# Optimization experiments

Hardware: AMD Instinct MI355X
Metric: run time of the kernel (lower is better)

Reference implementation:

```python
import jax, jax.numpy as jnp
import numpy as np

B, T, C, H = 8, 2048, 1024, 64  # batch, seq (== block_size), n_embd, head_size


def setup_inputs() -> dict:
    key = jax.random.key(0)
    k1, k2, k3, k4 = jax.random.split(key, 4)
    x = jax.random.normal(k1, (B, T, C), dtype=jnp.float32)
    scale = 0.02
    Wk = jax.random.normal(k2, (H, C), dtype=jnp.float32) * scale  # nn.Linear weight [out,in]
    Wq = jax.random.normal(k3, (H, C), dtype=jnp.float32) * scale
    Wv = jax.random.normal(k4, (H, C), dtype=jnp.float32) * scale
    return {"x": x, "Wk": Wk, "Wq": Wq, "Wv": Wv}


def reference(x, Wk, Wq, Wv):
    # k, q, v projections (bias-free linears): x @ W.T
    k = jnp.einsum('btc,hc->bth', x, Wk)
    q = jnp.einsum('btc,hc->bth', x, Wq)
    v = jnp.einsum('btc,hc->bth', x, Wv)
    # NOTE: source MULTIPLIES by sqrt(head_size) (faithful to original code)
    wei = jnp.einsum('bth,bsh->bts', q, k) * (H ** 0.5)  # [B,T,T]
    causal = jnp.tril(jnp.ones((T, T), dtype=bool))
    wei = jnp.where(causal, wei, -jnp.inf)
    wei = jax.nn.softmax(wei, axis=-1)
    # dropout_value = 0.0 -> identity (deterministic baseline)
    out = jnp.einsum('bts,bsh->bth', wei, v)  # [B,T,H]
    return out
```

## Files before the change

kernel.cpp:

```cpp
#include <hip/hip_runtime.h>

#define BB 8
#define TT 2048
#define CC 1024
#define HH 64
#define MM (BB * TT)

typedef _Float16 half8 __attribute__((ext_vector_type(8)));
typedef _Float16 half4 __attribute__((ext_vector_type(4)));
typedef float floatx4 __attribute__((ext_vector_type(4)));

template <int CTRL>
__device__ __forceinline__ float dpp_max_step(float x)
{
    union { float f; int i; } u, v;
    u.f = x;
    v.i = __builtin_amdgcn_update_dpp(u.i, u.i, CTRL, 0xf, 0xf, false);
    return fmaxf(x, v.f);
}
__device__ __forceinline__ float rowmax16(float x)
{
    x = dpp_max_step<0x128>(x);
    x = dpp_max_step<0x124>(x);
    x = dpp_max_step<0x122>(x);
    x = dpp_max_step<0x121>(x);
    return x;
}

__device__ __forceinline__ void gll16(const float* g, float* l)
{
    __builtin_amdgcn_global_load_lds(
        (const __attribute__((address_space(1))) unsigned int*)g,
        (__attribute__((address_space(3))) unsigned int*)l, 16, 0, 0);
}
__device__ __forceinline__ void gll16h(const _Float16* g, _Float16* l)
{
    __builtin_amdgcn_global_load_lds(
        (const __attribute__((address_space(1))) unsigned int*)g,
        (__attribute__((address_space(3))) unsigned int*)l, 16, 0, 0);
}

#define MEMFENCE asm volatile("" ::: "memory")

__global__ __launch_bounds__(256)
void w_pack(const float* __restrict__ Wk, const float* __restrict__ Wq,
            const float* __restrict__ Wv, _Float16* __restrict__ Wp)
{
    const int T   = blockIdx.x * 256 + threadIdx.x;
    const int c   = T / 768;
    const int rem = T - c * 768;
    const int nf  = rem >> 6;
    const int l   = rem & 63;
    const int col = nf * 16 + (l & 15);
    const int k   = c * 32 + (l >> 4) * 8;
    const int which = col >> 6;
    const float* __restrict__ src = (which == 0) ? Wq : ((which == 1) ? Wk : Wv);
    const float scale = (which == 0) ? 8.0f : 1.0f;
    const int srow = col & 63;
    const float4 a = *reinterpret_cast<const float4*>(&src[srow * 1024 + k]);
    const float4 b = *reinterpret_cast<const float4*>(&src[srow * 1024 + k + 4]);
    const half8 o = { (_Float16)(a.x * scale), (_Float16)(a.y * scale),
                      (_Float16)(a.z * scale), (_Float16)(a.w * scale),
                      (_Float16)(b.x * scale), (_Float16)(b.y * scale),
                      (_Float16)(b.z * scale), (_Float16)(b.w * scale) };
    *reinterpret_cast<half8*>(&Wp[(size_t)T * 8]) = o;
}

__global__ __launch_bounds__(512, 1)
void qkv12(const float* __restrict__ x, const _Float16* __restrict__ Wp,
           _Float16* __restrict__ q16, _Float16* __restrict__ Kp,
           _Float16* __restrict__ Vp)
{
    __shared__ float    xs[3][64][32];
    __shared__ _Float16 Ws[3][6144];

    const int tid  = threadIdx.x;
    const int lane = tid & 63;
    const int w    = tid >> 6;
    const int blk  = blockIdx.x;
    const int skew = blk & 31;
    const int m_base = blk * 64;
    const int fm = lane & 15;
    const int fq = lane >> 4;
    const int fk = fq * 8;
    const int fr = fq * 4;
    const int wm = w >> 2;
    const int wn = w & 3;

    const float* gsrc = &x[(size_t)(m_base + w * 8 + (lane >> 3)) * CC
                           + ((lane & 7) ^ (lane >> 3)) * 4];
    float* xbase = &xs[0][w * 8][0];

    const _Float16* wsrc = Wp + lane * 8;

    floatx4 acc[2][3];
    #pragma unroll
    for (int a = 0; a < 2; ++a)
        #pragma unroll
        for (int n = 0; n < 3; ++n)
            #pragma unroll
            for (int r = 0; r < 4; ++r) acc[a][n][r] = 0.0f;

#define STAGE_X(p, slot) gll16(gsrc + (size_t)(p) * 32, xbase + (slot) * 2048)
#define STAGE_W(p, slot) do {                                                  \
        const _Float16* wsp = wsrc + (size_t)(p) * 6144;                       \
        if (w < 4) {                                                           \
            gll16h(wsp + (2 * w) * 512,     &Ws[slot][(2 * w) * 512]);         \
            gll16h(wsp + (2 * w + 1) * 512, &Ws[slot][(2 * w + 1) * 512]);     \
        } else {                                                               \
            gll16h(wsp + (4 + w) * 512,     &Ws[slot][(4 + w) * 512]);         \
        }                                                                      \
    } while (0)

#define COMPUTE(sc) do {                                                       \
        const half8 wf0 = *reinterpret_cast<const half8*>(                     \
            &Ws[sc][(wn * 3 + 0) * 512 + lane * 8]);                           \
        const half8 wf1 = *reinterpret_cast<const half8*>(                     \
            &Ws[sc][(wn * 3 + 1) * 512 + lane * 8]);                           \
        const half8 wf2 = *reinterpret_cast<const half8*>(                     \
            &Ws[sc][(wn * 3 + 2) * 512 + lane * 8]);                           \
        _Pragma("unroll")                                                      \
        for (int a = 0; a < 2; ++a) {                                          \
            const float* rowp = &xs[sc][wm * 32 + a * 16 + fm][0];             \
            const int sw = fm & 7;                                             \
            const float4 v0 = *reinterpret_cast<const float4*>(                \
                rowp + ((fq * 2 + 0) ^ sw) * 4);                               \
            const float4 v1 = *reinterpret_cast<const float4*>(                \
                rowp + ((fq * 2 + 1) ^ sw) * 4);                               \
            const half8 af = { (_Float16)v0.x, (_Float16)v0.y,                 \
                               (_Float16)v0.z, (_Float16)v0.w,                 \
                               (_Float16)v1.x, (_Float16)v1.y,                 \
                               (_Float16)v1.z, (_Float16)v1.w };               \
            acc[a][0] = __builtin_amdgcn_mfma_f32_16x16x32_f16(af, wf0, acc[a][0], 0, 0, 0); \
            acc[a][1] = __builtin_amdgcn_mfma_f32_16x16x32_f16(af, wf1, acc[a][1], 0, 0, 0); \
            acc[a][2] = __builtin_amdgcn_mfma_f32_16x16x32_f16(af, wf2, acc[a][2], 0, 0, 0); \
        }                                                                      \
    } while (0)

#define WAITB(NLO, NHI) do {                                                   \
        if (w < 4) asm volatile("s_waitcnt vmcnt(" #NLO ")" ::: "memory");     \
        else       asm volatile("s_waitcnt vmcnt(" #NHI ")" ::: "memory");     \
        __builtin_amdgcn_s_barrier();                                          \
        MEMFENCE;                                                              \
    } while (0)

    MEMFENCE;
    STAGE_W(skew, 0);               STAGE_X(skew, 0);
    STAGE_W((skew + 1) & 31, 1);    STAGE_X((skew + 1) & 31, 1);
    WAITB(3, 2);

    for (int c = 0; c < 30; ++c) {
        const int pp = (c + 2 + skew) & 31;
        const int sl = (c + 2) % 3;
        STAGE_W(pp, sl);
        STAGE_X(pp, sl);
        MEMFENCE;
        COMPUTE(c % 3);
        WAITB(3, 2);
    }
    COMPUTE(0);
    WAITB(0, 0);
    COMPUTE(1);

#undef STAGE_X
#undef STAGE_W
#undef COMPUTE
#undef WAITB

    #pragma unroll
    for (int a = 0; a < 2; ++a) {
        const int mt = blk * 4 + wm * 2 + a;
        #pragma unroll
        for (int n = 0; n < 3; ++n) {
            const int col = wn * 48 + n * 16 + fm;
            if (col < 64) {
                #pragma unroll
                for (int r = 0; r < 4; ++r)
                    q16[(size_t)(mt * 16 + fr + r) * HH + col] = (_Float16)acc[a][n][r];
            } else if (col < 128) {
                const int h = col - 64;
                _Float16* kp = &Kp[(size_t)(mt * 2 + (h >> 5)) * 512 + (h & 31)];
                #pragma unroll
                for (int r = 0; r < 4; ++r)
                    kp[(fr + r) * 32] = (_Float16)acc[a][n][r];
            } else {
                const int h = col - 128;
                const half4 pk = { (_Float16)acc[a][n][0], (_Float16)acc[a][n][1],
                                   (_Float16)acc[a][n][2], (_Float16)acc[a][n][3] };
                *reinterpret_cast<half4*>(
                    &Vp[(size_t)((mt >> 2) * 4 + (h >> 4)) * 1024 +
                        ((mt >> 1) & 1) * 512 + fm * 32 + (mt & 1) * 16 + fr]) = pk;
            }
        }
    }
}

__global__ __launch_bounds__(256, 3)
void attn8(const _Float16* __restrict__ q16, const _Float16* __restrict__ Kp,
           const _Float16* __restrict__ Vp, float* __restrict__ out,
           _Float16* __restrict__ Op, float* __restrict__ ml)
{
    __shared__ _Float16 Kls[2][4][1024];
    __shared__ _Float16 Vls[2][4][1024];
    __shared__ _Float16 Ps[4][16 * 68];

    const int bid = blockIdx.x;
    const int g   = 31 - bid / 24;
    const int sub = bid - (31 - g) * 24;
    const int b   = sub & 7;
    const int s   = sub >> 3;

    const int tid  = threadIdx.x;
    const int lane = tid & 63;
    const int w    = tid >> 6;
    const int it   = g * 4 + w;
    const int fm = lane & 15;
    const int fq = lane >> 4;
    const int fk = fq * 8;
    const int fr = fq * 4;

    const int Ji = g + 1;
    const int qq = Ji / 3, rem = Ji - qq * 3;
    const int cnt   = qq + (s < rem ? 1 : 0);
    const int start = s * qq + (s < rem ? s : rem);

    const _Float16* __restrict__ kpb = Kp + (size_t)b * TT * HH;
    const _Float16* __restrict__ vpb = Vp + (size_t)b * TT * HH;

    const int qrow = (b * 128 + it) * 16 + fm;
    const half8 qf0 = *reinterpret_cast<const half8*>(&q16[(size_t)qrow * HH + fk]);
    const half8 qf1 = *reinterpret_cast<const half8*>(&q16[(size_t)qrow * HH + 32 + fk]);

    floatx4 O[4], lacc;
    float m_r[4];
    #pragma unroll
    for (int r = 0; r < 4; ++r) {
        m_r[r] = -3.0e38f;
        lacc[r] = 0.0f;
        #pragma unroll
        for (int ht = 0; ht < 4; ++ht) O[ht][r] = 0.0f;
    }
    const half8 ones = { (_Float16)1.f, (_Float16)1.f, (_Float16)1.f, (_Float16)1.f,
                         (_Float16)1.f, (_Float16)1.f, (_Float16)1.f, (_Float16)1.f };

    const int sperm = ((lane & 15) * 4 + (lane >> 4)) * 8;

    if (cnt > 0) {
        {
            const _Float16* kgp = &kpb[(size_t)(start * 4 + w) * 1024];
            const _Float16* vgp = &vpb[(size_t)(start * 4 + w) * 1024];
            gll16h(kgp + sperm,       &Kls[0][w][0]);
            gll16h(kgp + 512 + sperm, &Kls[0][w][512]);
            gll16h(vgp + sperm,       &Vls[0][w][0]);
            gll16h(vgp + 512 + sperm, &Vls[0][w][512]);
        }
        asm volatile("s_waitcnt vmcnt(0)" ::: "memory");
        __builtin_amdgcn_s_barrier();
        MEMFENCE;

        int buf = 0;
        for (int js = 0; js < cnt; ++js) {
            const int jj = start + js;

            if (js + 1 < cnt) {
                const _Float16* kgp = &kpb[(size_t)((jj + 1) * 4 + w) * 1024];
                const _Float16* vgp = &vpb[(size_t)((jj + 1) * 4 + w) * 1024];
                gll16h(kgp + sperm,       &Kls[buf ^ 1][w][0]);
                gll16h(kgp + 512 + sperm, &Kls[buf ^ 1][w][512]);
                gll16h(vgp + sperm,       &Vls[buf ^ 1][w][0]);
                gll16h(vgp + 512 + sperm, &Vls[buf ^ 1][w][512]);
            }
            MEMFENCE;

            floatx4 sa[4];
            #pragma unroll
            for (int nt = 0; nt < 4; ++nt) {
                #pragma unroll
                for (int r = 0; r < 4; ++r) sa[nt][r] = 0.0f;
                const half8 b0 = *reinterpret_cast<const half8*>(&Kls[buf][nt][lane * 8]);
                const half8 b1 = *reinterpret_cast<const half8*>(&Kls[buf][nt][512 + lane * 8]);
                sa[nt] = __builtin_amdgcn_mfma_f32_16x16x32_f16(qf0, b0, sa[nt], 0, 0, 0);
                sa[nt] = __builtin_amdgcn_mfma_f32_16x16x32_f16(qf1, b1, sa[nt], 0, 0, 0);
            }

            if (jj == g) {
                const int rbase = it * 16 + fr;
                #pragma unroll
                for (int nt = 0; nt < 4; ++nt) {
                    const int col = jj * 64 + nt * 16 + fm;
                    #pragma unroll
                    for (int r = 0; r < 4; ++r)
                        if (col > rbase + r) sa[nt][r] = -3.0e38f;
                }
            }

            #pragma unroll
            for (int r = 0; r < 4; ++r) {
                float mx = fmaxf(fmaxf(sa[0][r], sa[1][r]), fmaxf(sa[2][r], sa[3][r]));
                mx = rowmax16(mx);
                const float mn = fmaxf(m_r[r], mx);
                const float alpha = __expf(m_r[r] - mn);
                m_r[r] = mn;
                _Float16* pp = &Ps[w][(fr + r) * 68 + fm];
                pp[0]  = (_Float16)__expf(sa[0][r] - mn);
                pp[16] = (_Float16)__expf(sa[1][r] - mn);
                pp[32] = (_Float16)__expf(sa[2][r] - mn);
                pp[48] = (_Float16)__expf(sa[3][r] - mn);
                lacc[r] *= alpha;
                O[0][r] *= alpha; O[1][r] *= alpha; O[2][r] *= alpha; O[3][r] *= alpha;
            }

            #pragma unroll
            for (int ch = 0; ch < 2; ++ch) {
                const half8 pa = *reinterpret_cast<const half8*>(&Ps[w][fm * 68 + ch * 32 + fk]);
                lacc = __builtin_amdgcn_mfma_f32_16x16x32_f16(pa, ones, lacc, 0, 0, 0);
                #pragma unroll
                for (int ht = 0; ht < 4; ++ht) {
                    const half8 vb = *reinterpret_cast<const half8*>(
                        &Vls[buf][ht][ch * 512 + lane * 8]);
                    O[ht] = __builtin_amdgcn_mfma_f32_16x16x32_f16(pa, vb, O[ht], 0, 0, 0);
                }
            }

            asm volatile("s_waitcnt vmcnt(0)" ::: "memory");
            __builtin_amdgcn_s_barrier();
            MEMFENCE;
            buf ^= 1;
        }
    }

    #pragma unroll
    for (int r = 0; r < 4; ++r) {
        const int grow = (b * 128 + it) * 16 + fr + r;
        if (s == 0) {
            #pragma unroll
            for (int ht = 0; ht < 4; ++ht)
                out[(size_t)grow * HH + ht * 16 + fm] = O[ht][r];
        } else {
            #pragma unroll
            for (int ht = 0; ht < 4; ++ht)
                Op[((size_t)(s - 1) * MM + grow) * HH + ht * 16 + fm] = (_Float16)O[ht][r];
        }
        if (fm == 0) {
            ml[((size_t)s * MM + grow) * 2 + 0] = m_r[r];
            ml[((size_t)s * MM + grow) * 2 + 1] = lacc[r];
        }
    }
}

__global__ __launch_bounds__(256)
void combine(float* __restrict__ out, const _Float16* __restrict__ Op,
             const float* __restrict__ ml)
{
    const int tid  = threadIdx.x;
    const int grow = blockIdx.x * 64 + (tid >> 2);
    const int c0   = (tid & 3) * 16;

    const float m0 = ml[(size_t)grow * 2 + 0];
    const float l0 = ml[(size_t)grow * 2 + 1];
    const float m1 = ml[((size_t)MM + grow) * 2 + 0];
    const float l1 = ml[((size_t)MM + grow) * 2 + 1];
    const float m2 = ml[((size_t)2 * MM + grow) * 2 + 0];
    const float l2 = ml[((size_t)2 * MM + grow) * 2 + 1];

    const float M  = fmaxf(m0, fmaxf(m1, m2));
    const float w0 = __expf(m0 - M);
    const float w1 = __expf(m1 - M);
    const float w2 = __expf(m2 - M);
    const float inv = 1.0f / (w0 * l0 + w1 * l1 + w2 * l2);

    #pragma unroll
    for (int i = 0; i < 16; i += 4) {
        float4 o0 = *reinterpret_cast<float4*>(&out[(size_t)grow * HH + c0 + i]);
        const half4 h1 = *reinterpret_cast<const half4*>(&Op[(size_t)grow * HH + c0 + i]);
        const half4 h2 = *reinterpret_cast<const half4*>(&Op[(size_t)MM * HH + (size_t)grow * HH + c0 + i]);
        o0.x = (w0 * o0.x + w1 * (float)h1[0] + w2 * (float)h2[0]) * inv;
        o0.y = (w0 * o0.y + w1 * (float)h1[1] + w2 * (float)h2[1]) * inv;
        o0.z = (w0 * o0.z + w1 * (float)h1[2] + w2 * (float)h2[2]) * inv;
        o0.w = (w0 * o0.w + w1 * (float)h1[3] + w2 * (float)h2[3]) * inv;
        *reinterpret_cast<float4*>(&out[(size_t)grow * HH + c0 + i]) = o0;
    }
}

extern "C" void kernel_launch(void* const* d_in, const int* in_sizes, int n_in,
                              void* d_out, int out_size, void* d_ws, size_t ws_size,
                              hipStream_t stream)
{
    (void)in_sizes; (void)n_in; (void)out_size; (void)ws_size;

    const float* x  = (const float*)d_in[0];
    const float* Wk = (const float*)d_in[1];
    const float* Wq = (const float*)d_in[2];
    const float* Wv = (const float*)d_in[3];
    float* out = (float*)d_out;

    _Float16* base = (_Float16*)d_ws;
    _Float16* q16 = base;
    _Float16* Kp  = base + (size_t)MM * HH;
    _Float16* Vp  = base + (size_t)2 * MM * HH;
    _Float16* Wp  = base + (size_t)3 * MM * HH;
    _Float16* Op  = Wp + 192 * 1024;
    float*    ml  = (float*)(Op + (size_t)2 * MM * HH);

    w_pack<<<dim3(96), dim3(256), 0, stream>>>(Wk, Wq, Wv, Wp);
    qkv12<<<dim3(256), dim3(512), 0, stream>>>(x, Wp, q16, Kp, Vp);
    attn8<<<dim3(768), dim3(256), 0, stream>>>(q16, Kp, Vp, out, Op, ml);
    combine<<<dim3(256), dim3(256), 0, stream>>>(out, Op, ml);
}
```

Before: 146.9 us.

## Load x tiles directly into registers and double-buffer weights with 64-wide K steps

```diff
diff --git a/kernel.cpp b/kernel.cpp
--- a/kernel.cpp
+++ b/kernel.cpp
@@ -27,12 +27,6 @@
     return x;
 }
 
-__device__ __forceinline__ void gll16(const float* g, float* l)
-{
-    __builtin_amdgcn_global_load_lds(
-        (const __attribute__((address_space(1))) unsigned int*)g,
-        (__attribute__((address_space(3))) unsigned int*)l, 16, 0, 0);
-}
 __device__ __forceinline__ void gll16h(const _Float16* g, _Float16* l)
 {
     __builtin_amdgcn_global_load_lds(
@@ -67,18 +61,16 @@
 }
 
 __global__ __launch_bounds__(512, 1)
-void qkv12(const float* __restrict__ x, const _Float16* __restrict__ Wp,
+void qkv13(const float* __restrict__ x, const _Float16* __restrict__ Wp,
            _Float16* __restrict__ q16, _Float16* __restrict__ Kp,
            _Float16* __restrict__ Vp)
 {
-    __shared__ float    xs[3][64][32];
-    __shared__ _Float16 Ws[3][6144];
+    __shared__ _Float16 Ws[2][12288];
 
     const int tid  = threadIdx.x;
     const int lane = tid & 63;
     const int w    = tid >> 6;
     const int blk  = blockIdx.x;
-    const int skew = blk & 31;
     const int m_base = blk * 64;
     const int fm = lane & 15;
     const int fq = lane >> 4;
@@ -87,9 +79,8 @@
     const int wm = w >> 2;
     const int wn = w & 3;
 
-    const float* gsrc = &x[(size_t)(m_base + w * 8 + (lane >> 3)) * CC
-                           + ((lane & 7) ^ (lane >> 3)) * 4];
-    float* xbase = &xs[0][w * 8][0];
+    const float* xr0 = &x[(size_t)(m_base + wm * 32 + fm) * CC + fk];
+    const float* xr1 = xr0 + 16 * CC;
 
     const _Float16* wsrc = Wp + lane * 8;
 
@@ -101,71 +92,85 @@
             #pragma unroll
             for (int r = 0; r < 4; ++r) acc[a][n][r] = 0.0f;
 
-#define STAGE_X(p, slot) gll16(gsrc + (size_t)(p) * 32, xbase + (slot) * 2048)
-#define STAGE_W(p, slot) do {                                                  \
-        const _Float16* wsp = wsrc + (size_t)(p) * 6144;                       \
-        if (w < 4) {                                                           \
-            gll16h(wsp + (2 * w) * 512,     &Ws[slot][(2 * w) * 512]);         \
-            gll16h(wsp + (2 * w + 1) * 512, &Ws[slot][(2 * w + 1) * 512]);     \
-        } else {                                                               \
-            gll16h(wsp + (4 + w) * 512,     &Ws[slot][(4 + w) * 512]);         \
+    float4 xA[8], xB[8];
+
+#define STAGE_W(i, slot) do {                                                  \
+        const size_t fb = (size_t)(24 * (i) + 3 * w) * 512;                    \
+        gll16h(wsrc + fb,        &Ws[slot][(3 * w + 0) * 512]);                \
+        gll16h(wsrc + fb + 512,  &Ws[slot][(3 * w + 1) * 512]);                \
+        gll16h(wsrc + fb + 1024, &Ws[slot][(3 * w + 2) * 512]);                \
+    } while (0)
+
+#define LOAD_X(i, XB) do {                                                     \
+        _Pragma("unroll")                                                      \
+        for (int a = 0; a < 2; ++a) {                                          \
+            const float* xr = a ? xr1 : xr0;                                   \
+            _Pragma("unroll")                                                  \
+            for (int sub = 0; sub < 2; ++sub) {                                \
+                XB[a * 4 + sub * 2 + 0] = *reinterpret_cast<const float4*>(    \
+                    xr + (i) * 64 + sub * 32);                                 \
+                XB[a * 4 + sub * 2 + 1] = *reinterpret_cast<const float4*>(    \
+                    xr + (i) * 64 + sub * 32 + 4);                             \
+            }                                                                  \
         }                                                                      \
     } while (0)
 
-#define COMPUTE(sc) do {                                                       \
-        const half8 wf0 = *reinterpret_cast<const half8*>(                     \
-            &Ws[sc][(wn * 3 + 0) * 512 + lane * 8]);                           \
-        const half8 wf1 = *reinterpret_cast<const half8*>(                     \
-            &Ws[sc][(wn * 3 + 1) * 512 + lane * 8]);                           \
-        const half8 wf2 = *reinterpret_cast<const half8*>(                     \
-            &Ws[sc][(wn * 3 + 2) * 512 + lane * 8]);                           \
+#define COMPUTE(sl, XB) do {                                                   \
+        half8 wf[2][3];                                                        \
         _Pragma("unroll")                                                      \
-        for (int a = 0; a < 2; ++a) {                                          \
-            const float* rowp = &xs[sc][wm * 32 + a * 16 + fm][0];             \
-            const int sw = fm & 7;                                             \
-            const float4 v0 = *reinterpret_cast<const float4*>(                \
-                rowp + ((fq * 2 + 0) ^ sw) * 4);                               \
-            const float4 v1 = *reinterpret_cast<const float4*>(                \
-                rowp + ((fq * 2 + 1) ^ sw) * 4);                               \
-            const half8 af = { (_Float16)v0.x, (_Float16)v0.y,                 \
-                               (_Float16)v0.z, (_Float16)v0.w,                 \
-                               (_Float16)v1.x, (_Float16)v1.y,                 \
-                               (_Float16)v1.z, (_Float16)v1.w };               \
-            acc[a][0] = __builtin_amdgcn_mfma_f32_16x16x32_f16(af, wf0, acc[a][0], 0, 0, 0); \
-            acc[a][1] = __builtin_amdgcn_mfma_f32_16x16x32_f16(af, wf1, acc[a][1], 0, 0, 0); \
-            acc[a][2] = __builtin_amdgcn_mfma_f32_16x16x32_f16(af, wf2, acc[a][2], 0, 0, 0); \
-        }                                                                      \
+        for (int sub = 0; sub < 2; ++sub)                                      \
+            _Pragma("unroll")                                                  \
+            for (int n = 0; n < 3; ++n)                                        \
+                wf[sub][n] = *reinterpret_cast<const half8*>(                  \
+                    &Ws[sl][(sub * 12 + wn * 3 + n) * 512 + lane * 8]);        \
+        _Pragma("unroll")                                                      \
+        for (int a = 0; a < 2; ++a)                                            \
+            _Pragma("unroll")                                                  \
+            for (int sub = 0; sub < 2; ++sub) {                                \
+                const float4 v0 = XB[a * 4 + sub * 2 + 0];                     \
+                const float4 v1 = XB[a * 4 + sub * 2 + 1];                     \
+                const half8 af = { (_Float16)v0.x, (_Float16)v0.y,             \
+                                   (_Float16)v0.z, (_Float16)v0.w,             \
+                                   (_Float16)v1.x, (_Float16)v1.y,             \
+                                   (_Float16)v1.z, (_Float16)v1.w };           \
+                _Pragma("unroll")                                              \
+                for (int n = 0; n < 3; ++n)                                    \
+                    acc[a][n] = __builtin_amdgcn_mfma_f32_16x16x32_f16(        \
+                        af, wf[sub][n], acc[a][n], 0, 0, 0);                   \
+            }                                                                  \
     } while (0)
 
-#define WAITB(NLO, NHI) do {                                                   \
-        if (w < 4) asm volatile("s_waitcnt vmcnt(" #NLO ")" ::: "memory");     \
-        else       asm volatile("s_waitcnt vmcnt(" #NHI ")" ::: "memory");     \
+#define QITER(i, XC, XN) do {                                                  \
+        STAGE_W((i) + 1, ((i) + 1) & 1);                                       \
+        MEMFENCE;                        \
+        LOAD_X((i) + 1, XN);                                                   \
+        MEMFENCE;                                                              \
+        COMPUTE((i) & 1, XC);                                                  \
+        asm volatile("s_waitcnt vmcnt(8)" ::: "memory");                       \
         __builtin_amdgcn_s_barrier();                                          \
         MEMFENCE;                                                              \
     } while (0)
 
     MEMFENCE;
-    STAGE_W(skew, 0);               STAGE_X(skew, 0);
-    STAGE_W((skew + 1) & 31, 1);    STAGE_X((skew + 1) & 31, 1);
-    WAITB(3, 2);
-
-    for (int c = 0; c < 30; ++c) {
-        const int pp = (c + 2 + skew) & 31;
-        const int sl = (c + 2) % 3;
-        STAGE_W(pp, sl);
-        STAGE_X(pp, sl);
-        MEMFENCE;
-        COMPUTE(c % 3);
-        WAITB(3, 2);
-    }
-    COMPUTE(0);
-    WAITB(0, 0);
-    COMPUTE(1);
-
-#undef STAGE_X
+    STAGE_W(0, 0);
+    MEMFENCE;
+    LOAD_X(0, xA);
+    MEMFENCE;
+    asm volatile("s_waitcnt vmcnt(8)" ::: "memory");
+    __builtin_amdgcn_s_barrier();
+    MEMFENCE;
+
+    for (int ii = 0; ii < 7; ++ii) {
+        QITER(2 * ii,     xA, xB);
+        QITER(2 * ii + 1, xB, xA);
+    }
+    QITER(14, xA, xB);
+    COMPUTE(1, xB);
+
 #undef STAGE_W
+#undef LOAD_X
 #undef COMPUTE
-#undef WAITB
+#undef QITER
 
     #pragma unroll
     for (int a = 0; a < 2; ++a) {
@@ -403,7 +408,7 @@
     float*    ml  = (float*)(Op + (size_t)2 * MM * HH);
 
     w_pack<<<dim3(96), dim3(256), 0, stream>>>(Wk, Wq, Wv, Wp);
-    qkv12<<<dim3(256), dim3(512), 0, stream>>>(x, Wp, q16, Kp, Vp);
+    qkv13<<<dim3(256), dim3(512), 0, stream>>>(x, Wp, q16, Kp, Vp);
     attn8<<<dim3(768), dim3(256), 0, stream>>>(q16, Kp, Vp, out, Op, ml);
     combine<<<dim3(256), dim3(256), 0, stream>>>(out, Op, ml);
 }
```

Measured after the change: 147.1 us. No clear change (+0.2%).
